# Kernel optimization log

Measured on AMD Instinct MI355X. Metric: run time of the kernel, lower is better.

The kernel has to match this reference:

```python
import jax, jax.numpy as jnp
import numpy as np

# dims
B, T, H = 4, 2048, 768
HEADS, D = 4, 768          # GATConv(out_channels=768, heads=4, concat=False)
L = 3                      # num_layers
WIN = 2
K = 2 * WIN + 1
EPS = 1e-5
NEG_SLOPE = 0.2            # PyG GATConv leaky_relu slope


def setup_inputs() -> dict:
    key = jax.random.key(0)
    ks = jax.random.split(key, 4)
    s = 1.0 / np.sqrt(H)
    x = jax.random.normal(ks[0], (B, T, H), jnp.float32)
    W = jax.random.normal(ks[1], (L, H, HEADS, D), jnp.float32) * s   # lin weights per layer
    a_src = jax.random.normal(ks[2], (L, HEADS, D), jnp.float32) * s  # att_src
    a_dst = jax.random.normal(ks[3], (L, HEADS, D), jnp.float32) * s  # att_dst
    bias = jnp.zeros((L, D), jnp.float32)                             # GATConv bias (concat=False -> [D])
    gamma = jnp.ones((L, H), jnp.float32)                             # LayerNorm weight
    beta = jnp.zeros((L, H), jnp.float32)                             # LayerNorm bias
    return {"x": x, "W": W, "a_src": a_src, "a_dst": a_dst,
            "bias": bias, "gamma": gamma, "beta": beta}


def _layernorm(z, g, b):
    m = jnp.mean(z, axis=-1, keepdims=True)
    v = jnp.mean((z - m) ** 2, axis=-1, keepdims=True)
    return (z - m) * jax.lax.rsqrt(v + EPS) * g + b


def _gat_layer(x, Wl, asrc_w, adst_w, bias_l, idx, mask):
    # x: [B,T,H]; banded GAT with neighborhoods idx: [T,K] (clipped), mask: [T,K]
    h = jnp.einsum('bti,ihd->bthd', x, Wl)                 # [B,T,heads,D]
    asrc = jnp.einsum('bthd,hd->bth', h, asrc_w)           # per-source-node score term
    adst = jnp.einsum('bthd,hd->bth', h, adst_w)           # per-target-node score term
    h_nb = h[:, idx]                                       # [B,T,K,heads,D] gathered neighbors j
    score = jax.nn.leaky_relu(asrc[:, idx] + adst[:, :, None, :], NEG_SLOPE)  # [B,T,K,heads]
    score = jnp.where(mask[None, :, :, None], score, -jnp.inf)
    attn = jax.nn.softmax(score, axis=2)                   # softmax over incoming edges per target
    out = jnp.einsum('btkh,btkhd->bthd', attn, h_nb)       # weighted aggregation
    return out.mean(axis=2) + bias_l                       # concat=False -> mean over heads


def reference(x, W, a_src, a_dst, bias, gamma, beta):
    # banded neighborhood indices (window edges both directions + self-loop from PyG default)
    offs = jnp.arange(-WIN, WIN + 1)
    idx = jnp.arange(T)[:, None] + offs[None, :]           # [T,K]
    mask = (idx >= 0) & (idx < T)
    idx = jnp.clip(idx, 0, T - 1)
    for l in range(L):
        res = x
        y = _gat_layer(x, W[l], a_src[l], a_dst[l], bias[l], idx, mask)
        x = _layernorm(y + res, gamma[l], beta[l])         # dropout = identity in eval
    return x
```

## Files before the change

### kernel.cpp

```cpp
#include <hip/hip_runtime.h>
#include <stdint.h>

#define TT 2048
#define BB 4
#define HH 768
#define NHEADS 4
#define DD 768
#define NN 3072
#define LL 3
#define BT 8192
#define KNB 5
#define NBLK 12
#define ATPB 4
#define NROWS 8

typedef __bf16 bf16x8 __attribute__((ext_vector_type(8)));
typedef float f32x4 __attribute__((ext_vector_type(4)));

__device__ __forceinline__ unsigned short f2bf(float f){
  union { float f; unsigned u; } v; v.f = f;
  unsigned u = v.u;
  return (unsigned short)((u + 0x7FFFu + ((u >> 16) & 1u)) >> 16);
}
__device__ __forceinline__ float bf2f(unsigned short h){
  union { unsigned u; float f; } v; v.u = ((unsigned)h) << 16;
  return v.f;
}
__device__ __forceinline__ void gload16(const unsigned short* g, unsigned short* l){
  __builtin_amdgcn_global_load_lds((const __attribute__((address_space(1))) void*)g,
                                   (__attribute__((address_space(3))) void*)l, 16, 0, 0);
}

__global__ void wt_kernel(const float* __restrict__ W, unsigned short* __restrict__ Wt){
  __shared__ float tile[32][33];
  int l = blockIdx.z;
  int n0 = blockIdx.x * 32, k0 = blockIdx.y * 32;
  int tx = threadIdx.x, ty = threadIdx.y;
  const float* Wl = W + (size_t)l * HH * NN;
  for (int r = 0; r < 4; r++)
    tile[ty + r*8][tx] = Wl[(size_t)(k0 + ty + r*8) * NN + n0 + tx];
  __syncthreads();
  unsigned short* Wtl = Wt + (size_t)l * NN * HH;
  for (int r = 0; r < 4; r++){
    int n = n0 + ty + r*8;
    Wtl[(size_t)n * HH + k0 + tx] = f2bf(tile[tx][ty + r*8]);
  }
}

__global__ void xconv_kernel(const float* __restrict__ x, unsigned short* __restrict__ xb){
  int i = blockIdx.x * blockDim.x + threadIdx.x;
  float4 v = ((const float4*)x)[i];
  ushort4 o;
  o.x = f2bf(v.x); o.y = f2bf(v.y); o.z = f2bf(v.z); o.w = f2bf(v.w);
  *(ushort4*)(xb + (size_t)i * 4) = o;
}

#define BM 128
#define BN 128
#define BK 64

__global__ __launch_bounds__(256, 2) void gemm_kernel(
    const unsigned short* __restrict__ xb,
    const unsigned short* __restrict__ wt,
    unsigned short* __restrict__ hout,
    const float* __restrict__ a_srcl,
    const float* __restrict__ a_dstl,
    float* __restrict__ psrc,
    float* __restrict__ pdst){
  __shared__ __align__(16) unsigned short xs[BM][BK];
  __shared__ __align__(16) unsigned short wsd[BN][BK];
  int bm = blockIdx.y * BM;
  int bn = blockIdx.x * BN;
  int tid = threadIdx.x;
  int wave = tid >> 6, lane = tid & 63;
  int m16 = lane & 15, q = lane >> 4;
  int wm = (wave >> 1) * 64, wn = (wave & 1) * 64;
  int r8 = lane >> 3, c8 = lane & 7;
  int cg = (c8 ^ r8) * 8;
  const unsigned short* ga[4]; const unsigned short* gb[4];
  unsigned short* la[4]; unsigned short* lb[4];
  #pragma unroll
  for (int s = 0; s < 4; s++){
    int row = wave * 32 + s * 8;
    ga[s] = xb + (size_t)(bm + row + r8) * HH + cg;
    gb[s] = wt + (size_t)(bn + row + r8) * HH + cg;
    la[s] = &xs[row][0];
    lb[s] = &wsd[row][0];
  }
  int rd0 = ((0 + q) ^ (m16 & 7)) * 8;
  int rd1 = ((4 + q) ^ (m16 & 7)) * 8;
  f32x4 acc[4][4] = {};
  for (int k0 = 0; k0 < HH; k0 += BK){
    #pragma unroll
    for (int s = 0; s < 4; s++){
      gload16(ga[s] + k0, la[s]);
      gload16(gb[s] + k0, lb[s]);
    }
    __syncthreads();
    bf16x8 af[4], bfr[4];
    for (int i = 0; i < 4; i++)
      af[i] = __builtin_bit_cast(bf16x8, *(const uint4*)(&xs[wm + i*16 + m16][rd0]));
    for (int j = 0; j < 4; j++)
      bfr[j] = __builtin_bit_cast(bf16x8, *(const uint4*)(&wsd[wn + j*16 + m16][rd0]));
    for (int i = 0; i < 4; i++)
      for (int j = 0; j < 4; j++)
        acc[i][j] = __builtin_amdgcn_mfma_f32_16x16x32_bf16(af[i], bfr[j], acc[i][j], 0, 0, 0);
    for (int i = 0; i < 4; i++)
      af[i] = __builtin_bit_cast(bf16x8, *(const uint4*)(&xs[wm + i*16 + m16][rd1]));
    for (int j = 0; j < 4; j++)
      bfr[j] = __builtin_bit_cast(bf16x8, *(const uint4*)(&wsd[wn + j*16 + m16][rd1]));
    for (int i = 0; i < 4; i++)
      for (int j = 0; j < 4; j++)
        acc[i][j] = __builtin_amdgcn_mfma_f32_16x16x32_bf16(af[i], bfr[j], acc[i][j], 0, 0, 0);
    __syncthreads();
  }
  for (int i = 0; i < 4; i++){
    int row0 = bm + wm + i*16 + q*4;
    for (int j = 0; j < 4; j++){
      int col = bn + wn + j*16 + m16;
      unsigned short* hp = hout + (size_t)row0 * NN + col;
      hp[0]            = f2bf(acc[i][j][0]);
      hp[NN]           = f2bf(acc[i][j][1]);
      hp[2*(size_t)NN] = f2bf(acc[i][j][2]);
      hp[3*(size_t)NN] = f2bf(acc[i][j][3]);
    }
  }
  int col0 = bn + wn;
  int head = col0 / DD;
  int blk  = (col0 % DD) >> 6;
  float wsrc[4], wdstw[4];
  for (int j = 0; j < 4; j++){
    int n = col0 + j*16 + m16;
    wsrc[j]  = a_srcl[n];
    wdstw[j] = a_dstl[n];
  }
  for (int i = 0; i < 4; i++){
    for (int reg = 0; reg < 4; reg++){
      float ss = 0.f, dd = 0.f;
      for (int j = 0; j < 4; j++){
        float v = acc[i][j][reg];
        ss += v * wsrc[j];
        dd += v * wdstw[j];
      }
      ss += __shfl_xor(ss, 1, 64); dd += __shfl_xor(dd, 1, 64);
      ss += __shfl_xor(ss, 2, 64); dd += __shfl_xor(dd, 2, 64);
      ss += __shfl_xor(ss, 4, 64); dd += __shfl_xor(dd, 4, 64);
      ss += __shfl_xor(ss, 8, 64); dd += __shfl_xor(dd, 8, 64);
      if (m16 == 0){
        int row = bm + wm + i*16 + q*4 + reg;
        size_t slot = (size_t)row * (NHEADS * NBLK) + head * NBLK + blk;
        psrc[slot] = ss;
        pdst[slot] = dd;
      }
    }
  }
}

__global__ __launch_bounds__(256) void srcred_kernel(
    const float* __restrict__ psrc, const float* __restrict__ pdst,
    float* __restrict__ asrc, float* __restrict__ adst){
  int task = blockIdx.x * 256 + threadIdx.x;
  const float* ps = psrc + (size_t)task * NBLK;
  const float* pd = pdst + (size_t)task * NBLK;
  float ss = 0.f, dd = 0.f;
  for (int i = 0; i < NBLK; i++){ ss += ps[i]; dd += pd[i]; }
  asrc[task] = ss;
  adst[task] = dd;
}

__global__ __launch_bounds__(384) void attn_ln_kernel(const unsigned short* __restrict__ h,
    const float* __restrict__ asrc, const float* __restrict__ adst,
    const float* __restrict__ x_in, const float* __restrict__ bias_l,
    const float* __restrict__ gamma_l, const float* __restrict__ beta_l,
    float* __restrict__ x_out, unsigned short* __restrict__ xb_next){
  int bid = blockIdx.x;
  int grp = ((bid & 7) << 8) | (bid >> 3);
  int token0 = grp * ATPB;
  int t0 = token0 & (TT - 1);
  int bseq = token0 >> 11;
  int tid = threadIdx.x;
  int wave = tid >> 6, lane = tid & 63;
  __shared__ __align__(16) unsigned short hs[NROWS][NN];
  __shared__ float attn_s[ATPB][NHEADS][KNB];
  __shared__ float part_s[ATPB * 96], part_q[ATPB * 96];
  __shared__ float mv_mean[ATPB], mv_rstd[ATPB];
  #pragma unroll
  for (int j = 0; j < NROWS; j++){
    int g = t0 - 2 + j;
    g = min(max(g, 0), TT - 1);
    const unsigned short* src = h + ((size_t)(bseq * TT + g)) * NN + tid * 8;
    gload16(src, &hs[j][wave * 512]);
  }
  if (tid < ATPB * NHEADS){
    int ti = tid >> 2, head = tid & 3;
    int token = token0 + ti, t = t0 + ti;
    float sc[KNB];
    float mx = -3.0e38f;
    float ad = adst[token * NHEADS + head];
    for (int k = 0; k < KNB; k++){
      int tn = t + k - 2;
      if (tn >= 0 && tn < TT){
        float s = asrc[(token + k - 2) * NHEADS + head] + ad;
        s = s > 0.f ? s : 0.2f * s;
        sc[k] = s; mx = fmaxf(mx, s);
      } else sc[k] = -3.0e38f;
    }
    float den = 0.f;
    for (int k = 0; k < KNB; k++){
      float e = (sc[k] > -1.0e38f) ? __expf(sc[k] - mx) : 0.f;
      sc[k] = e; den += e;
    }
    float inv = 0.25f / den;
    for (int k = 0; k < KNB; k++) attn_s[ti][head][k] = sc[k] * inv;
  }
  __syncthreads();
  int ti = tid / 96, c = tid % 96;
  int token = token0 + ti;
  float ac[NHEADS][KNB];
  for (int hd = 0; hd < NHEADS; hd++)
    for (int k = 0; k < KNB; k++) ac[hd][k] = attn_s[ti][hd][k];
  float y8[8] = {};
  for (int hd = 0; hd < NHEADS; hd++){
    #pragma unroll
    for (int k = 0; k < KNB; k++){
      bf16x8 v = __builtin_bit_cast(bf16x8, *(const uint4*)(&hs[ti + k][hd * DD + c * 8]));
      float a = ac[hd][k];
      #pragma unroll
      for (int e = 0; e < 8; e++) y8[e] += a * (float)v[e];
    }
  }
  float xr[8], bb[8];
  { const float4* p = (const float4*)&x_in[(size_t)token * HH + c * 8];
    *(float4*)&xr[0] = p[0]; *(float4*)&xr[4] = p[1]; }
  { const float4* p = (const float4*)&bias_l[c * 8];
    *(float4*)&bb[0] = p[0]; *(float4*)&bb[4] = p[1]; }
  float s = 0.f, sq = 0.f;
  #pragma unroll
  for (int e = 0; e < 8; e++){
    float zz = y8[e] + bb[e] + xr[e];
    y8[e] = zz; s += zz; sq += zz * zz;
  }
  part_s[tid] = s; part_q[tid] = sq;
  __syncthreads();
  if (wave < ATPB){
    float vs = part_s[wave * 96 + lane];
    float vq = part_q[wave * 96 + lane];
    if (lane < 32){
      vs += part_s[wave * 96 + 64 + lane];
      vq += part_q[wave * 96 + 64 + lane];
    }
    for (int off = 32; off > 0; off >>= 1){
      vs += __shfl_xor(vs, off, 64);
      vq += __shfl_xor(vq, off, 64);
    }
    if (lane == 0){
      float mean = vs * (1.f / HH);
      float var = vq * (1.f / HH) - mean * mean;
      mv_mean[wave] = mean;
      mv_rstd[wave] = rsqrtf(var + 1e-5f);
    }
  }
  __syncthreads();
  float mean = mv_mean[ti], rstd = mv_rstd[ti];
  float gr[8], br[8];
  { const float4* p = (const float4*)&gamma_l[c * 8];
    *(float4*)&gr[0] = p[0]; *(float4*)&gr[4] = p[1]; }
  { const float4* p = (const float4*)&beta_l[c * 8];
    *(float4*)&br[0] = p[0]; *(float4*)&br[4] = p[1]; }
  float o[8];
  unsigned short o16[8];
  #pragma unroll
  for (int e = 0; e < 8; e++){
    o[e] = (y8[e] - mean) * rstd * gr[e] + br[e];
    o16[e] = f2bf(o[e]);
  }
  float* xo = &x_out[(size_t)token * HH + c * 8];
  *(float4*)&xo[0] = *(float4*)&o[0];
  *(float4*)&xo[4] = *(float4*)&o[4];
  *(uint4*)(&xb_next[(size_t)token * HH + c * 8]) = *(uint4*)&o16[0];
}

extern "C" void kernel_launch(void* const* d_in, const int* in_sizes, int n_in,
                              void* d_out, int out_size, void* d_ws, size_t ws_size,
                              hipStream_t stream) {
  const float* x     = (const float*)d_in[0];
  const float* W     = (const float*)d_in[1];
  const float* a_src = (const float*)d_in[2];
  const float* a_dst = (const float*)d_in[3];
  const float* bias  = (const float*)d_in[4];
  const float* gamma = (const float*)d_in[5];
  const float* beta  = (const float*)d_in[6];
  float* out = (float*)d_out;

  char* ws = (char*)d_ws;
  size_t off = 0;
  auto alloc = [&](size_t bytes)->char*{
    char* p = ws + off;
    off = (off + bytes + 255) & ~(size_t)255;
    return p;
  };
  unsigned short* wt   = (unsigned short*)alloc((size_t)LL * NN * HH * 2);
  unsigned short* xb   = (unsigned short*)alloc((size_t)BT * HH * 2);
  unsigned short* hbuf = (unsigned short*)alloc((size_t)BT * NN * 2);
  float* psrc  = (float*)alloc((size_t)BT * NHEADS * NBLK * 4);
  float* pdst  = (float*)alloc((size_t)BT * NHEADS * NBLK * 4);
  float* asrcb = (float*)alloc((size_t)BT * NHEADS * 4);
  float* adstb = (float*)alloc((size_t)BT * NHEADS * 4);

  wt_kernel<<<dim3(NN/32, HH/32, LL), dim3(32, 8), 0, stream>>>(W, wt);
  xconv_kernel<<<(BT * HH / 4) / 256, 256, 0, stream>>>(x, xb);

  for (int l = 0; l < LL; l++){
    const float* xin = (l == 0) ? x : out;
    gemm_kernel<<<dim3(NN / BN, BT / BM), 256, 0, stream>>>(
        xb, wt + (size_t)l * NN * HH, hbuf,
        a_src + (size_t)l * NHEADS * DD, a_dst + (size_t)l * NHEADS * DD,
        psrc, pdst);
    srcred_kernel<<<BT * NHEADS / 256, 256, 0, stream>>>(psrc, pdst, asrcb, adstb);
    attn_ln_kernel<<<BT / ATPB, 384, 0, stream>>>(hbuf, asrcb, adstb, xin,
        bias + (size_t)l * DD, gamma + (size_t)l * HH, beta + (size_t)l * HH,
        out, xb);
  }
}
```

Baseline: 340.1 us.

## Widen attention blocks to 8 tokens, read bf16 residual, skip unneeded output writes

The attention+LayerNorm kernel now handles 8 tokens per block with 768 threads. It loads 12 halo-padded h rows into a padded LDS buffer instead of 8 rows for 4 tokens, which cuts the redundant neighbor-row reloads from global memory. Intermediate layers take the residual from the bf16 activation buffer instead of the fp32 output. Each layer then writes only what the next consumer needs: bf16 for the next GEMM, or fp32 on the final layer. This lowers memory traffic, but the residual path is rounded to bf16, which adds some numerical error.

```diff
diff --git a/kernel.cpp b/kernel.cpp
--- a/kernel.cpp
+++ b/kernel.cpp
@@ -11,8 +11,9 @@
 #define BT 8192
 #define KNB 5
 #define NBLK 12
-#define ATPB 4
-#define NROWS 8
+#define ATPB 8
+#define NROWS 12
+#define HSTR 3080
 
 typedef __bf16 bf16x8 __attribute__((ext_vector_type(8)));
 typedef float f32x4 __attribute__((ext_vector_type(4)));
@@ -168,28 +169,33 @@
   adst[task] = dd;
 }
 
-__global__ __launch_bounds__(384) void attn_ln_kernel(const unsigned short* __restrict__ h,
+__global__ __launch_bounds__(768) void attn_ln_kernel(const unsigned short* __restrict__ h,
     const float* __restrict__ asrc, const float* __restrict__ adst,
-    const float* __restrict__ x_in, const float* __restrict__ bias_l,
+    const float* __restrict__ xin_f32,
+    const unsigned short* __restrict__ xin_bf,
+    const float* __restrict__ bias_l,
     const float* __restrict__ gamma_l, const float* __restrict__ beta_l,
-    float* __restrict__ x_out, unsigned short* __restrict__ xb_next){
+    float* __restrict__ x_out, unsigned short* __restrict__ xb_next,
+    int write_f32){
   int bid = blockIdx.x;
-  int grp = ((bid & 7) << 8) | (bid >> 3);
+  int grp = ((bid & 7) << 7) | (bid >> 3);
   int token0 = grp * ATPB;
   int t0 = token0 & (TT - 1);
   int bseq = token0 >> 11;
   int tid = threadIdx.x;
   int wave = tid >> 6, lane = tid & 63;
-  __shared__ __align__(16) unsigned short hs[NROWS][NN];
+  __shared__ __align__(16) unsigned short hs[NROWS][HSTR];
   __shared__ float attn_s[ATPB][NHEADS][KNB];
   __shared__ float part_s[ATPB * 96], part_q[ATPB * 96];
   __shared__ float mv_mean[ATPB], mv_rstd[ATPB];
+  int wv6 = wave % 6, jh = wave / 6;
   #pragma unroll
-  for (int j = 0; j < NROWS; j++){
+  for (int it = 0; it < 6; it++){
+    int j = it * 2 + jh;
     int g = t0 - 2 + j;
     g = min(max(g, 0), TT - 1);
-    const unsigned short* src = h + ((size_t)(bseq * TT + g)) * NN + tid * 8;
-    gload16(src, &hs[j][wave * 512]);
+    const unsigned short* src = h + ((size_t)(bseq * TT + g)) * NN + wv6 * 512 + lane * 8;
+    gload16(src, &hs[j][wv6 * 512]);
   }
   if (tid < ATPB * NHEADS){
     int ti = tid >> 2, head = tid & 3;
@@ -230,8 +236,15 @@
     }
   }
   float xr[8], bb[8];
-  { const float4* p = (const float4*)&x_in[(size_t)token * HH + c * 8];
-    *(float4*)&xr[0] = p[0]; *(float4*)&xr[4] = p[1]; }
+  if (xin_f32){
+    const float4* p = (const float4*)&xin_f32[(size_t)token * HH + c * 8];
+    *(float4*)&xr[0] = p[0]; *(float4*)&xr[4] = p[1];
+  } else {
+    uint4 u = *(const uint4*)&xin_bf[(size_t)token * HH + c * 8];
+    const unsigned short* us = (const unsigned short*)&u;
+    #pragma unroll
+    for (int e = 0; e < 8; e++) xr[e] = bf2f(us[e]);
+  }
   { const float4* p = (const float4*)&bias_l[c * 8];
     *(float4*)&bb[0] = p[0]; *(float4*)&bb[4] = p[1]; }
   float s = 0.f, sq = 0.f;
@@ -268,16 +281,19 @@
   { const float4* p = (const float4*)&beta_l[c * 8];
     *(float4*)&br[0] = p[0]; *(float4*)&br[4] = p[1]; }
   float o[8];
-  unsigned short o16[8];
   #pragma unroll
-  for (int e = 0; e < 8; e++){
+  for (int e = 0; e < 8; e++)
     o[e] = (y8[e] - mean) * rstd * gr[e] + br[e];
-    o16[e] = f2bf(o[e]);
-  }
-  float* xo = &x_out[(size_t)token * HH + c * 8];
-  *(float4*)&xo[0] = *(float4*)&o[0];
-  *(float4*)&xo[4] = *(float4*)&o[4];
-  *(uint4*)(&xb_next[(size_t)token * HH + c * 8]) = *(uint4*)&o16[0];
+  if (write_f32){
+    float* xo = &x_out[(size_t)token * HH + c * 8];
+    *(float4*)&xo[0] = *(float4*)&o[0];
+    *(float4*)&xo[4] = *(float4*)&o[4];
+  } else {
+    unsigned short o16[8];
+    #pragma unroll
+    for (int e = 0; e < 8; e++) o16[e] = f2bf(o[e]);
+    *(uint4*)(&xb_next[(size_t)token * HH + c * 8]) = *(uint4*)&o16[0];
+  }
 }
 
 extern "C" void kernel_launch(void* const* d_in, const int* in_sizes, int n_in,
@@ -311,14 +327,14 @@
   xconv_kernel<<<(BT * HH / 4) / 256, 256, 0, stream>>>(x, xb);
 
   for (int l = 0; l < LL; l++){
-    const float* xin = (l == 0) ? x : out;
     gemm_kernel<<<dim3(NN / BN, BT / BM), 256, 0, stream>>>(
         xb, wt + (size_t)l * NN * HH, hbuf,
         a_src + (size_t)l * NHEADS * DD, a_dst + (size_t)l * NHEADS * DD,
         psrc, pdst);
     srcred_kernel<<<BT * NHEADS / 256, 256, 0, stream>>>(psrc, pdst, asrcb, adstb);
-    attn_ln_kernel<<<BT / ATPB, 384, 0, stream>>>(hbuf, asrcb, adstb, xin,
+    attn_ln_kernel<<<BT / ATPB, 768, 0, stream>>>(hbuf, asrcb, adstb,
+        (l == 0) ? x : nullptr, xb,
         bias + (size_t)l * DD, gamma + (size_t)l * HH, beta + (size_t)l * HH,
-        out, xb);
-  }
-}
+        out, xb, (l == LL - 1) ? 1 : 0);
+  }
+}
```

Measured after the change: 346.2 us. About the same (+1.8%).
